# Kernel optimization log

Hardware: AMD Instinct MI355X
Metric: run time of the kernel (lower is better)

The kernel has to match this reference:

```python
import jax, jax.numpy as jnp
import numpy as np

HEADS = 16
NUM_LANDMARKS = 64
PINV_ITERS = 6
D_MODEL = 1024


def _moore_penrose_pinv(x, num_iters):
    # Newton-Schulz iteration: V <- 0.25*V @ (13I - KV @ (15I - KV @ (7I - KV)))
    m = x.shape[-1]
    I = jnp.eye(m, dtype=x.dtype)
    V = x
    for _ in range(num_iters):
        KV = x @ V  # [..., m, m]
        V = 0.25 * V @ (13.0 * I - KV @ (15.0 * I - KV @ (7.0 * I - KV)))
    return V


def setup_inputs() -> dict:
    key = jax.random.key(0)
    k1, k2, k3 = jax.random.split(key, 3)
    b, n, d = 4, 4096, D_MODEL
    hidden_states = jax.random.normal(k1, (b, n, d), dtype=jnp.float32)
    Wqkv = jax.random.normal(k2, (d, 3 * d), dtype=jnp.float32) * 0.02
    bqkv = jnp.zeros((3 * d,), dtype=jnp.float32)
    Wout = jax.random.normal(k3, (d, d), dtype=jnp.float32) * 0.02
    bout = jnp.zeros((d,), dtype=jnp.float32)
    return {"hidden_states": hidden_states, "Wqkv": Wqkv, "bqkv": bqkv,
            "Wout": Wout, "bout": bout}


def reference(hidden_states, Wqkv, bqkv, Wout, bout):
    b, n, d = hidden_states.shape
    h, m = HEADS, NUM_LANDMARKS
    dh = d // h
    scale = 1.0 / np.sqrt(dh).astype(np.float32)
    # n is a multiple of m by construction, so the torch padding branch is a no-op.
    l = n // m  # tokens per landmark group

    qkv = hidden_states @ Wqkv + bqkv  # [b, n, 3d]
    q, k, v = jnp.split(qkv, 3, axis=-1)

    def to_heads(t):  # [b, n, d] -> [b, h, n, dh]
        return t.reshape(b, n, h, dh).transpose(0, 2, 1, 3)

    q, k, v = to_heads(q), to_heads(k), to_heads(v)
    q = q * scale

    # Landmarks: mean over contiguous groups of l tokens (sum / l in original).
    q_l = q.reshape(b, h, m, l, dh).mean(axis=3)  # [b, h, m, dh]
    k_l = k.reshape(b, h, m, l, dh).mean(axis=3)

    sim1 = jnp.einsum('bhid,bhjd->bhij', q, k_l)    # [b, h, n, m]
    sim2 = jnp.einsum('bhid,bhjd->bhij', q_l, k_l)  # [b, h, m, m]
    sim3 = jnp.einsum('bhid,bhjd->bhij', q_l, k)    # [b, h, m, n]

    attn1 = jax.nn.softmax(sim1, axis=-1)
    attn2 = jax.nn.softmax(sim2, axis=-1)
    attn3 = jax.nn.softmax(sim3, axis=-1)

    attn2_inv = _moore_penrose_pinv(attn2, PINV_ITERS)

    # out = attn1 @ attn2_inv @ (attn3 @ v), cheapest association
    out = attn1 @ (attn2_inv @ (attn3 @ v))  # [b, h, n, dh]
    out = out.transpose(0, 2, 1, 3).reshape(b, n, d)
    out = out @ Wout + bout
    return out
```

## Files before the change

### kernel.cpp

```cpp
#include <hip/hip_runtime.h>
#include <cstdint>

typedef unsigned short u16;
typedef __attribute__((ext_vector_type(8))) short s16x8;
typedef __attribute__((ext_vector_type(4))) float f32x4;

#define NTOK 4096
#define DH   64
#define DM   1024
#define NH   16

static __device__ __forceinline__ float b2f(u16 u){ return __uint_as_float(((unsigned)u)<<16); }
static __device__ __forceinline__ u16 f2b(float f){
  unsigned u = __float_as_uint(f);
  return (u16)((u + 0x7FFFu + ((u>>16)&1u)) >> 16);
}

static __device__ __forceinline__ void gload_lds16(const void* g, void* l) {
  __builtin_amdgcn_global_load_lds(
      (const __attribute__((address_space(1))) unsigned*)(uintptr_t)g,
      (__attribute__((address_space(3))) unsigned*)(uintptr_t)l, 16, 0, 0);
}

static __device__ __forceinline__ s16x8 ld8(const u16* p){ return *(const s16x8*)(const void*)p; }

__global__ __launch_bounds__(256) void k_pre(const float* __restrict__ hs, u16* __restrict__ Xb,
                                             float* __restrict__ Xl,
                                             const float* __restrict__ Wqkv, u16* __restrict__ WqkvT,
                                             const float* __restrict__ Wout, u16* __restrict__ WoutT) {
  __shared__ float tile[64][65];
  const int bid = blockIdx.x, t = threadIdx.x;
  if (bid < 1024) {
    const int grp = bid >> 2;
    const int d = (bid & 3)*256 + t;
    const float* p = hs + (long)grp*64*DM + d;
    u16* xo = Xb + (long)grp*64*DM + d;
    float s = 0.f;
    #pragma unroll 8
    for (int i = 0; i < 64; ++i) {
      const float v = p[(long)i*DM];
      s += v;
      xo[(long)i*DM] = f2b(v);
    }
    Xl[(long)grp*DM + d] = s * (1.0f/64.0f);
    return;
  }
  const float* in; u16* out; int R, C, tc, tr;
  if (bid < 1792) { const int x = bid - 1024; in = Wqkv; out = WqkvT; R = 1024; C = 3072; tc = x % 48; tr = x / 48; }
  else            { const int x = bid - 1792; in = Wout; out = WoutT; R = 1024; C = 1024; tc = x & 15;  tr = x >> 4; }
  const int cx = t & 63, ry = t >> 6;
  #pragma unroll
  for (int p = 0; p < 16; ++p) {
    const int row = p*4 + ry;
    tile[row][cx] = in[(long)(tr*64 + row)*C + tc*64 + cx];
  }
  __syncthreads();
  #pragma unroll
  for (int p = 0; p < 16; ++p) {
    const int orow = p*4 + ry;
    out[(long)(tc*64 + orow)*R + tr*64 + cx] = f2b(tile[cx][orow]);
  }
}

__global__ __launch_bounds__(256) void k_lproj2(const float* __restrict__ Xl, const float* __restrict__ Wqkv,
                                                float* __restrict__ psum) {
  __shared__ __align__(16) float Xs[32][68];
  const int t = threadIdx.x;
  const int wcol = blockIdx.x*256 + t;
  const int r0 = blockIdx.y*32;
  const int kbase = blockIdx.z*128;
  float acc[32];
  #pragma unroll
  for (int r = 0; r < 32; ++r) acc[r] = 0.f;
  for (int k0 = kbase; k0 < kbase + 128; k0 += 64) {
    __syncthreads();
    for (int idx = t; idx < 2048; idx += 256)
      Xs[idx>>6][idx&63] = Xl[(long)(r0 + (idx>>6))*DM + k0 + (idx&63)];
    __syncthreads();
    for (int kk = 0; kk < 64; kk += 4) {
      f32x4 wv;
      #pragma unroll
      for (int j = 0; j < 4; ++j) wv[j] = Wqkv[(long)(k0+kk+j)*3072 + wcol];
      #pragma unroll
      for (int r = 0; r < 32; ++r) {
        const f32x4 xv = *(const f32x4*)&Xs[r][kk];
        acc[r] += xv[0]*wv[0] + xv[1]*wv[1] + xv[2]*wv[2] + xv[3]*wv[3];
      }
    }
  }
  float* po = psum + ((long)blockIdx.z*256 + r0)*2048 + wcol;
  #pragma unroll
  for (int r = 0; r < 32; ++r) po[(long)r*2048] = acc[r];
}

__global__ __launch_bounds__(256) void k_lreduce(const float* __restrict__ psum, const float* __restrict__ bqkv,
                                                 float* __restrict__ qlf, float* __restrict__ klf,
                                                 u16* __restrict__ qlb, u16* __restrict__ klb) {
  const long idx = (long)blockIdx.x*256 + threadIdx.x;
  const int row = (int)(idx >> 11), col = (int)(idx & 2047);
  float s = 0.f;
  #pragma unroll
  for (int z = 0; z < 8; ++z) s += psum[((long)z*256 + row)*2048 + col];
  const int isq = (col < 1024) ? 1 : 0;
  float val = s + bqkv[col];
  if (isq) val *= 0.125f;
  const int b = row >> 6, lm = row & 63;
  const int c2 = col & 1023, h = c2 >> 6, dh = c2 & 63;
  const long o = (((long)b*NH + h)*64 + lm)*64 + dh;
  if (isq) { qlf[o] = val; qlb[o] = f2b(val); }
  else     { klf[o] = val; klb[o] = f2b(val); }
}

template<int EPI>
__global__ __launch_bounds__(512, 2) void k_gemm256(
    const u16* __restrict__ A, const u16* __restrict__ Bt, const float* __restrict__ bias,
    int N, float* __restrict__ outF, u16* __restrict__ outQ, u16* __restrict__ outK, u16* __restrict__ outV)
{
  __shared__ __align__(16) u16 lds[2*32768];
  const int t = threadIdx.x;
  const int lane = t & 63;
  const int wid = t >> 6;
  const int c = lane & 15, g = lane >> 4;
  const int wm = wid >> 2, wn = wid & 3;
  const int fid = blockIdx.y*64 + blockIdx.x;
  const int nbx = ((fid & 7) << 3) | ((fid >> 3) & 7);
  const int nby = fid >> 6;
  const long arow0 = (long)nbx * 256;
  const long brow0 = (long)nby * 256;
  char* ldsb = (char*)lds;

  const int srow3 = t >> 3;
  const int sch = ((t & 7) ^ (srow3 & 7)) * 8;
  const u16* sA = A  + (arow0 + srow3)*1024 + sch;
  const u16* sB = Bt + (brow0 + srow3)*1024 + sch;
  const int dbase = t*16;

#define STG(gp, R0, Toff, kbe, nb) { \
    char* d0 = ldsb + (nb)*65536 + (Toff) + (R0)*128 + dbase; \
    gload_lds16((gp) + (long)(R0)*1024 + (kbe), d0); \
    gload_lds16((gp) + (long)((R0)+64)*1024 + (kbe), d0 + 8192); }

  const int cp0 = ((g     ) ^ (c & 7)) * 16;
  const int cp1 = ((4 | g ) ^ (c & 7)) * 16;
  int rowA[4], rowB[4];
  #pragma unroll
  for (int mi = 0; mi < 4; ++mi) {
    rowA[mi] = (wm*64 + mi*16 + c)*128;
    rowB[mi] = 32768 + (wn*64 + mi*16 + c)*128;
  }

  f32x4 acc0[4][4] = {};
  f32x4 acc1[4][4] = {};

  STG(sB, 0, 32768, 0, 0)
  STG(sB, 128, 32768, 0, 0)
  STG(sA, 0, 0, 0, 0)
  STG(sA, 128, 0, 0, 0)
  asm volatile("s_waitcnt vmcnt(2)" ::: "memory");
  __builtin_amdgcn_s_barrier();

  for (int it = 0; it < 16; ++it) {
    char* buf = ldsb + (it&1)*65536;
    const int nb = (it+1)&1;
    const int kb1 = (it+1)*64;
    const bool last = (it == 15);
    s16x8 fa[4], fb[4], ga[4];
    #pragma unroll
    for (int mi = 0; mi < 4; ++mi) fa[mi] = *(const s16x8*)(buf + rowA[mi] + cp0);
    #pragma unroll
    for (int ni = 0; ni < 4; ++ni) fb[ni] = *(const s16x8*)(buf + rowB[ni] + cp0);
    if (!last) STG(sB, 0, 32768, kb1, nb)
    __builtin_amdgcn_s_barrier();
    asm volatile("s_waitcnt lgkmcnt(0)" ::: "memory");
    __builtin_amdgcn_sched_barrier(0);
    __builtin_amdgcn_s_setprio(1);
    #pragma unroll
    for (int mi = 0; mi < 4; ++mi)
      #pragma unroll
      for (int ni = 0; ni < 4; ++ni)
        acc0[mi][ni] = __builtin_amdgcn_mfma_f32_16x16x32_bf16(fa[mi], fb[ni], acc0[mi][ni], 0, 0, 0);
    __builtin_amdgcn_s_setprio(0);
    if (last) { asm volatile("s_waitcnt vmcnt(0)" ::: "memory"); }
    else      { asm volatile("s_waitcnt vmcnt(2)" ::: "memory"); }
    __builtin_amdgcn_s_barrier();
    #pragma unroll
    for (int mi = 0; mi < 4; ++mi) ga[mi] = *(const s16x8*)(buf + rowA[mi] + 16384 + cp0);
    if (!last) STG(sB, 128, 32768, kb1, nb)
    __builtin_amdgcn_s_barrier();
    asm volatile("s_waitcnt lgkmcnt(0)" ::: "memory");
    __builtin_amdgcn_sched_barrier(0);
    __builtin_amdgcn_s_setprio(1);
    #pragma unroll
    for (int mi = 0; mi < 4; ++mi)
      #pragma unroll
      for (int ni = 0; ni < 4; ++ni)
        acc1[mi][ni] = __builtin_amdgcn_mfma_f32_16x16x32_bf16(ga[mi], fb[ni], acc1[mi][ni], 0, 0, 0);
    __builtin_amdgcn_s_setprio(0);
    __builtin_amdgcn_s_barrier();
    #pragma unroll
    for (int mi = 0; mi < 4; ++mi) fa[mi] = *(const s16x8*)(buf + rowA[mi] + cp1);
    #pragma unroll
    for (int ni = 0; ni < 4; ++ni) fb[ni] = *(const s16x8*)(buf + rowB[ni] + cp1);
    if (!last) STG(sA, 0, 0, kb1, nb)
    __builtin_amdgcn_s_barrier();
    asm volatile("s_waitcnt lgkmcnt(0)" ::: "memory");
    __builtin_amdgcn_sched_barrier(0);
    __builtin_amdgcn_s_setprio(1);
    #pragma unroll
    for (int mi = 0; mi < 4; ++mi)
      #pragma unroll
      for (int ni = 0; ni < 4; ++ni)
        acc0[mi][ni] = __builtin_amdgcn_mfma_f32_16x16x32_bf16(fa[mi], fb[ni], acc0[mi][ni], 0, 0, 0);
    __builtin_amdgcn_s_setprio(0);
    __builtin_amdgcn_s_barrier();
    #pragma unroll
    for (int mi = 0; mi < 4; ++mi) ga[mi] = *(const s16x8*)(buf + rowA[mi] + 16384 + cp1);
    if (!last) STG(sA, 128, 0, kb1, nb)
    __builtin_amdgcn_s_barrier();
    asm volatile("s_waitcnt lgkmcnt(0)" ::: "memory");
    __builtin_amdgcn_sched_barrier(0);
    __builtin_amdgcn_s_setprio(1);
    #pragma unroll
    for (int mi = 0; mi < 4; ++mi)
      #pragma unroll
      for (int ni = 0; ni < 4; ++ni)
        acc1[mi][ni] = __builtin_amdgcn_mfma_f32_16x16x32_bf16(ga[mi], fb[ni], acc1[mi][ni], 0, 0, 0);
    __builtin_amdgcn_s_setprio(0);
    if (!last) { asm volatile("s_waitcnt vmcnt(2)" ::: "memory"); }
    __builtin_amdgcn_s_barrier();
  }
#undef STG

  if (EPI == 0) {
    const int tensor = (int)(brow0 >> 10);
    if (tensor == 2) {
      __syncthreads();
      u16* wlds = lds + wid*4224;
      const int hbase = (int)((brow0 + wn*64) & 1023);
      const int head = hbase >> 6;
      #pragma unroll
      for (int ph = 0; ph < 2; ++ph) {
        const long grow0 = arow0 + ph*128 + wm*64;
        const int b = (int)(grow0 >> 12), tok0r = (int)(grow0 & 4095);
        #pragma unroll
        for (int mi = 0; mi < 4; ++mi)
          #pragma unroll
          for (int ni = 0; ni < 4; ++ni) {
            const float bv = bias[brow0 + wn*64 + ni*16 + c];
            const f32x4 a = ph ? acc1[mi][ni] : acc0[mi][ni];
            #pragma unroll
            for (int r = 0; r < 4; ++r)
              wlds[(mi*16 + g*4 + r)*66 + ni*16 + c] = f2b(a[r] + bv);
          }
        asm volatile("s_waitcnt lgkmcnt(0)" ::: "memory");
        u16* vbase = outV + (((long)b*NH + head)*DH)*NTOK + tok0r;
        #pragma unroll
        for (int j = 0; j < 8; ++j) {
          const int d = j*8 + (lane >> 3);
          const int tk = (lane & 7)*8;
          s16x8 vv;
          #pragma unroll
          for (int s2 = 0; s2 < 8; ++s2) vv[s2] = (short)wlds[(tk + s2)*66 + d];
          *(s16x8*)(vbase + (long)d*NTOK + tk) = vv;
        }
        asm volatile("s_waitcnt lgkmcnt(0)" ::: "memory");
      }
    } else {
      u16* dst = (tensor == 0) ? outQ : outK;
      const float mul = (tensor == 0) ? 0.125f : 1.0f;
      #pragma unroll
      for (int ph = 0; ph < 2; ++ph)
        #pragma unroll
        for (int mi = 0; mi < 4; ++mi) {
          const int rowb = ph*128 + wm*64 + mi*16 + g*4;
          #pragma unroll
          for (int ni = 0; ni < 4; ++ni) {
            const long gcol = brow0 + wn*64 + ni*16 + c;
            const int c2 = (int)(gcol & 1023);
            const int head = c2 >> 6, dh = c2 & 63;
            const float bv = bias[gcol];
            const f32x4 a = ph ? acc1[mi][ni] : acc0[mi][ni];
            #pragma unroll
            for (int r = 0; r < 4; ++r) {
              const long grow = arow0 + rowb + r;
              const int b = (int)(grow >> 12), tok = (int)(grow & 4095);
              dst[(((long)b*NH + head)*NTOK + tok)*DH + dh] = f2b((a[r] + bv)*mul);
            }
          }
        }
    }
  } else {
    #pragma unroll
    for (int ph = 0; ph < 2; ++ph)
      #pragma unroll
      for (int mi = 0; mi < 4; ++mi) {
        const int rowb = ph*128 + wm*64 + mi*16 + g*4;
        #pragma unroll
        for (int ni = 0; ni < 4; ++ni) {
          const long gcol = brow0 + wn*64 + ni*16 + c;
          const float bv = bias[gcol];
          const f32x4 a = ph ? acc1[mi][ni] : acc0[mi][ni];
          #pragma unroll
          for (int r = 0; r < 4; ++r) {
            const long grow = arow0 + rowb + r;
            outF[grow*N + gcol] = a[r] + bv;
          }
        }
      }
  }
}

#define PST 68
static __device__ __forceinline__ void mm_nn8(const float* A, const float* B, float* C, int t) {
  const int lane = t & 63, j0 = (t >> 6) << 3;
  float acc[8];
  #pragma unroll
  for (int j = 0; j < 8; ++j) acc[j] = 0.f;
  for (int k = 0; k < 64; k += 4) {
    const f32x4 a4 = *(const f32x4*)&A[lane*PST + k];
    #pragma unroll
    for (int dk = 0; dk < 4; ++dk) {
      const float a = a4[dk];
      const float* br = &B[(k + dk)*PST + j0];
      const f32x4 b0 = *(const f32x4*)(br);
      const f32x4 b1 = *(const f32x4*)(br + 4);
      #pragma unroll
      for (int qq = 0; qq < 4; ++qq) { acc[qq] += a*b0[qq]; acc[4+qq] += a*b1[qq]; }
    }
  }
  #pragma unroll
  for (int j = 0; j < 8; ++j) C[lane*PST + j0 + j] = acc[j];
}
static __device__ __forceinline__ void mm_nt8(const float* A, const float* B, float* C, int t) {
  const int lane = t & 63, j0 = (t >> 6) << 3;
  float acc[8];
  #pragma unroll
  for (int j = 0; j < 8; ++j) acc[j] = 0.f;
  for (int k = 0; k < 64; k += 4) {
    const f32x4 a4 = *(const f32x4*)&A[lane*PST + k];
    #pragma unroll
    for (int jj = 0; jj < 8; ++jj) {
      const f32x4 b4 = *(const f32x4*)&B[(j0 + jj)*PST + k];
      acc[jj] += a4[0]*b4[0] + a4[1]*b4[1] + a4[2]*b4[2] + a4[3]*b4[3];
    }
  }
  #pragma unroll
  for (int j = 0; j < 8; ++j) C[lane*PST + j0 + j] = acc[j];
}
static __device__ __forceinline__ void mm_nn4(const float* A, const float* B, float* C, int t) {
  const int lane = t & 63, j0 = (t >> 6) << 2;
  float acc[4] = {0.f, 0.f, 0.f, 0.f};
  for (int k = 0; k < 64; k += 4) {
    const f32x4 a4 = *(const f32x4*)&A[lane*PST + k];
    #pragma unroll
    for (int dk = 0; dk < 4; ++dk) {
      const f32x4 b0 = *(const f32x4*)&B[(k + dk)*PST + j0];
      #pragma unroll
      for (int q = 0; q < 4; ++q) acc[q] += a4[dk]*b0[q];
    }
  }
  #pragma unroll
  for (int j = 0; j < 4; ++j) C[lane*PST + j0 + j] = acc[j];
}

__global__ __launch_bounds__(512) void k_pa(const float* __restrict__ qlf, const float* __restrict__ klf,
                                            float* __restrict__ a2inv,
                                            const u16* __restrict__ qlb, const u16* __restrict__ kk,
                                            const u16* __restrict__ vt,
                                            float* __restrict__ zp, float* __restrict__ sp) {
  __shared__ __align__(16) char smem[87040];
  const int t = threadIdx.x;
  if (blockIdx.x < 64) {
    float* Xb = (float*)smem;
    float* Vb = Xb + 64*PST;
    float* T1 = Vb + 64*PST;
    float* T2 = T1 + 64*PST;
    float* T3 = T2 + 64*PST;
    const int bh = blockIdx.x;
    const float* ql = qlf + (long)bh*4096;
    const float* kl = klf + (long)bh*4096;
    for (int i = t; i < 4096; i += 512) { T1[(i>>6)*PST + (i&63)] = ql[i]; T2[(i>>6)*PST + (i&63)] = kl[i]; }
    __syncthreads();
    mm_nt8(T1, T2, Xb, t);
    __syncthreads();
    if (t < 64) {
      float mx = -1e30f;
      for (int j = 0; j < 64; ++j) mx = fmaxf(mx, Xb[t*PST + j]);
      float s = 0.f;
      for (int j = 0; j < 64; ++j) { const float e = expf(Xb[t*PST + j] - mx); Xb[t*PST + j] = e; s += e; }
      const float inv = 1.0f/s;
      for (int j = 0; j < 64; ++j) Xb[t*PST + j] *= inv;
    }
    __syncthreads();
    for (int i = t; i < 4096; i += 512) { const int r = i>>6, cc = i&63; Vb[r*PST+cc] = Xb[r*PST+cc]; }
    __syncthreads();
    for (int it = 0; it < 6; ++it) {
      mm_nn8(Xb, Vb, T1, t);  __syncthreads();
      for (int i = t; i < 4096; i += 512) { const int r=i>>6, cc=i&63; T2[r*PST+cc] = (r==cc?7.0f:0.0f) - T1[r*PST+cc]; }
      __syncthreads();
      mm_nn8(T1, T2, T3, t);  __syncthreads();
      for (int i = t; i < 4096; i += 512) { const int r=i>>6, cc=i&63; T2[r*PST+cc] = (r==cc?15.0f:0.0f) - T3[r*PST+cc]; }
      __syncthreads();
      mm_nn8(T1, T2, T3, t);  __syncthreads();
      for (int i = t; i < 4096; i += 512) { const int r=i>>6, cc=i&63; T2[r*PST+cc] = (r==cc?13.0f:0.0f) - T3[r*PST+cc]; }
      __syncthreads();
      mm_nn8(Vb, T2, T3, t);  __syncthreads();
      for (int i = t; i < 4096; i += 512) { const int r=i>>6, cc=i&63; Vb[r*PST+cc] = 0.25f*T3[r*PST+cc]; }
      __syncthreads();
    }
    for (int i = t; i < 4096; i += 512) a2inv[(long)bh*4096 + i] = Vb[(i>>6)*PST + (i&63)];
    return;
  }
  float* Zlp = (float*)smem;
  float* Slp = (float*)(smem + 65536);
  char*  Plb = smem + 66560;
  const int abid = blockIdx.x - 64;
  const int bh = abid >> 3, qt = abid & 7;
  if (t < 256) {
    const int w = t >> 6, lane = t & 63;
    const int c = lane & 15, g = lane >> 4;
    s16x8 aq[4][2];
    const u16* qlp = qlb + (long)bh*4096;
    #pragma unroll
    for (int mi = 0; mi < 4; ++mi)
      #pragma unroll
      for (int ks = 0; ks < 2; ++ks)
        aq[mi][ks] = ld8(qlp + (mi*16 + c)*64 + ks*32 + g*8);

    f32x4 zacc[4][4] = {};
    float sl[4][4] = {};
    const u16* kp = kk + (long)bh*NTOK*DH;
    const u16* vp = vt + (long)bh*DH*NTOK;
    char* pbase = Plb + w*5120;
    const int tok00 = qt*512 + w*128;

    for (int it = 0; it < 4; ++it) {
      const int t0 = tok00 + it*32;
      f32x4 sacc[4][2] = {};
      s16x8 kb[2][2];
      #pragma unroll
      for (int cg = 0; cg < 2; ++cg)
        #pragma unroll
        for (int ks = 0; ks < 2; ++ks)
          kb[cg][ks] = ld8(kp + (long)(t0 + cg*16 + c)*64 + ks*32 + g*8);
      #pragma unroll
      for (int cg = 0; cg < 2; ++cg)
        #pragma unroll
        for (int ks = 0; ks < 2; ++ks)
          #pragma unroll
          for (int mi = 0; mi < 4; ++mi)
            sacc[mi][cg] = __builtin_amdgcn_mfma_f32_16x16x32_bf16(aq[mi][ks], kb[cg][ks], sacc[mi][cg], 0, 0, 0);
      #pragma unroll
      for (int mi = 0; mi < 4; ++mi)
        #pragma unroll
        for (int r = 0; r < 4; ++r) {
          const int row = mi*16 + g*4 + r;
          const float p0 = __expf(sacc[mi][0][r]);
          const float p1 = __expf(sacc[mi][1][r]);
          sl[mi][r] += p0 + p1;
          char* base = pbase + row*80;
          *(u16*)(base + c*2)      = f2b(p0);
          *(u16*)(base + 32 + c*2) = f2b(p1);
        }
      s16x8 pa[4];
      #pragma unroll
      for (int mi = 0; mi < 4; ++mi) pa[mi] = *(const s16x8*)(pbase + (mi*16 + c)*80 + g*16);
      #pragma unroll
      for (int ni = 0; ni < 4; ++ni) {
        const s16x8 vb = ld8(vp + (long)(ni*16 + c)*NTOK + t0 + g*8);
        #pragma unroll
        for (int mi = 0; mi < 4; ++mi)
          zacc[mi][ni] = __builtin_amdgcn_mfma_f32_16x16x32_bf16(pa[mi], vb, zacc[mi][ni], 0, 0, 0);
      }
    }
    #pragma unroll
    for (int mi = 0; mi < 4; ++mi)
      #pragma unroll
      for (int r = 0; r < 4; ++r) {
        float s = sl[mi][r];
        s += __shfl_xor(s, 1); s += __shfl_xor(s, 2); s += __shfl_xor(s, 4); s += __shfl_xor(s, 8);
        sl[mi][r] = s;
      }
    #pragma unroll
    for (int mi = 0; mi < 4; ++mi)
      #pragma unroll
      for (int ni = 0; ni < 4; ++ni)
        #pragma unroll
        for (int r = 0; r < 4; ++r)
          Zlp[w*4096 + (mi*16 + g*4 + r)*64 + ni*16 + c] = zacc[mi][ni][r];
    if (c == 0)
      #pragma unroll
      for (int mi = 0; mi < 4; ++mi)
        #pragma unroll
        for (int r = 0; r < 4; ++r)
          Slp[w*64 + mi*16 + g*4 + r] = sl[mi][r];
  }
  __syncthreads();
  float* zpp = zp + (long)abid*4096;
  for (int i = t; i < 4096; i += 512)
    zpp[i] = Zlp[i] + Zlp[4096 + i] + Zlp[8192 + i] + Zlp[12288 + i];
  if (t < 64) sp[(long)abid*64 + t] = Slp[t] + Slp[64 + t] + Slp[128 + t] + Slp[192 + t];
}

__global__ __launch_bounds__(1024) void k_w2(const float* __restrict__ a2inv,
                                             const float* __restrict__ zp, const float* __restrict__ sp,
                                             u16* __restrict__ w2t) {
  __shared__ __align__(16) float Ai[64*PST];
  __shared__ __align__(16) float Zi[64*PST];
  __shared__ __align__(16) float Ci[64*PST];
  __shared__ float Ss[64];
  const int bh = blockIdx.x, t = threadIdx.x;
  if (t < 64) {
    float ss = 0.f;
    #pragma unroll
    for (int qt = 0; qt < 8; ++qt) ss += sp[(long)(bh*8 + qt)*64 + t];
    Ss[t] = 1.0f / ss;
  }
  for (int i = t; i < 4096; i += 1024)
    Ai[(i>>6)*PST + (i&63)] = a2inv[(long)bh*4096 + i];
  __syncthreads();
  for (int i = t; i < 4096; i += 1024) {
    float zs = 0.f;
    #pragma unroll
    for (int qt = 0; qt < 8; ++qt) zs += zp[((long)(bh*8 + qt))*4096 + i];
    Zi[(i>>6)*PST + (i&63)] = zs * Ss[i>>6];
  }
  __syncthreads();
  mm_nn4(Ai, Zi, Ci, t);
  __syncthreads();
  for (int i = t; i < 4096; i += 1024) { const int r = i>>6, cc = i&63; w2t[(long)bh*4096 + cc*64 + r] = f2b(Ci[r*PST + cc]); }
}

#define P1ST 144
__global__ __launch_bounds__(256) void k_attn1(const u16* __restrict__ q, const u16* __restrict__ klb,
                                               const u16* __restrict__ w2t, u16* __restrict__ ao) {
  __shared__ __align__(16) u16 Pl[4][64][72];
  const int bx = blockIdx.x, bh = bx >> 4, tt = bx & 15;
  const int b = bh >> 4, h = bh & 15;
  const int t = threadIdx.x, w = t >> 6, lane = t & 63;
  const int c = lane & 15, g = lane >> 4;
  const int tok0 = tt*256 + w*64;
  const u16* qp  = q + ((long)bh*NTOK + tok0)*DH;
  const u16* klp = klb + (long)bh*4096;
  const u16* wp  = w2t + (long)bh*4096;
  char* pbase = (char*)&Pl[w][0][0];

  s16x8 aq[4][2], kb[4][2], wb[4][2];
  #pragma unroll
  for (int i = 0; i < 4; ++i)
    #pragma unroll
    for (int ks = 0; ks < 2; ++ks) {
      aq[i][ks] = ld8(qp + (long)(i*16 + c)*DH + ks*32 + g*8);
      kb[i][ks] = ld8(klp + (i*16 + c)*64 + ks*32 + g*8);
      wb[i][ks] = ld8(wp  + (i*16 + c)*64 + ks*32 + g*8);
    }
  f32x4 sacc[4][4] = {};
  #pragma unroll
  for (int ks = 0; ks < 2; ++ks)
    #pragma unroll
    for (int mi = 0; mi < 4; ++mi)
      #pragma unroll
      for (int ni = 0; ni < 4; ++ni)
        sacc[mi][ni] = __builtin_amdgcn_mfma_f32_16x16x32_bf16(aq[mi][ks], kb[ni][ks], sacc[mi][ni], 0, 0, 0);

  float rs[4][4];
  #pragma unroll
  for (int mi = 0; mi < 4; ++mi)
    #pragma unroll
    for (int r = 0; r < 4; ++r) {
      const int row = mi*16 + g*4 + r;
      char* base = pbase + row*P1ST;
      float ssum = 0.f;
      #pragma unroll
      for (int ni = 0; ni < 4; ++ni) {
        const float p = __expf(sacc[mi][ni][r]);
        ssum += p;
        *(u16*)(base + (ni*16 + c)*2) = f2b(p);
      }
      ssum += __shfl_xor(ssum, 1); ssum += __shfl_xor(ssum, 2);
      ssum += __shfl_xor(ssum, 4); ssum += __shfl_xor(ssum, 8);
      rs[mi][r] = ssum;
    }
  __builtin_amdgcn_s_barrier();
  s16x8 pa[4][2];
  #pragma unroll
  for (int mi = 0; mi < 4; ++mi)
    #pragma unroll
    for (int ks = 0; ks < 2; ++ks)
      pa[mi][ks] = *(const s16x8*)(pbase + (mi*16 + c)*P1ST + ks*64 + g*16);
  f32x4 oacc[4][4] = {};
  #pragma unroll
  for (int ks = 0; ks < 2; ++ks)
    #pragma unroll
    for (int mi = 0; mi < 4; ++mi)
      #pragma unroll
      for (int ni = 0; ni < 4; ++ni)
        oacc[mi][ni] = __builtin_amdgcn_mfma_f32_16x16x32_bf16(pa[mi][ks], wb[ni][ks], oacc[mi][ni], 0, 0, 0);

  u16* op = ao + (long)b*NTOK*DM + (long)h*64;
  #pragma unroll
  for (int mi = 0; mi < 4; ++mi)
    #pragma unroll
    for (int r = 0; r < 4; ++r) {
      const int tok = tok0 + mi*16 + g*4 + r;
      const float inv = 1.0f / rs[mi][r];
      #pragma unroll
      for (int ni = 0; ni < 4; ++ni)
        op[(long)tok*DM + ni*16 + c] = f2b(oacc[mi][ni][r] * inv);
    }
}

extern "C" void kernel_launch(void* const* d_in, const int* in_sizes, int n_in,
                              void* d_out, int out_size, void* d_ws, size_t ws_size,
                              hipStream_t stream) {
  const float* hs   = (const float*)d_in[0];
  const float* Wqkv = (const float*)d_in[1];
  const float* bqkv = (const float*)d_in[2];
  const float* Wout = (const float*)d_in[3];
  const float* bout = (const float*)d_in[4];
  float* out = (float*)d_out;
  char* w = (char*)d_ws;

  u16*  Xb    = (u16*)(w);
  float* zp   = (float*)(w);
  float* sp   = (float*)(w + 8388608L);
  u16*  WqkvT = (u16*)(w + 33554432L);
  u16*  WoutT = (u16*)(w + 39845888L);
  u16*  q     = (u16*)(w + 41943040L);
  float* psum = (float*)(w + 41943040L);
  u16*  k     = (u16*)(w + 75497472L);
  float* Xl   = (float*)(w + 109051904L);
  u16*  vt    = (u16*)(w + 142606336L);
  float* qlf  = (float*)(w + 176160768L);
  float* klf  = (float*)(w + 177209344L);
  u16*  qlb   = (u16*)(w + 178257920L);
  u16*  klb   = (u16*)(w + 178782208L);
  float* a2i  = (float*)(w + 179306496L);
  u16*  w2t   = (u16*)(w + 181403648L);
  u16*  ao    = (u16*)(w + 181927936L);

  k_pre<<<2048, 256, 0, stream>>>(hs, Xb, Xl, Wqkv, WqkvT, Wout, WoutT);
  k_lproj2<<<dim3(8,8,8), 256, 0, stream>>>(Xl, Wqkv, psum);
  k_lreduce<<<2048, 256, 0, stream>>>(psum, bqkv, qlf, klf, qlb, klb);
  k_gemm256<0><<<dim3(64,12), 512, 0, stream>>>(Xb, WqkvT, bqkv, 3072, nullptr, q, k, vt);
  k_pa<<<576, 512, 0, stream>>>(qlf, klf, a2i, qlb, k, vt, zp, sp);
  k_w2<<<64, 1024, 0, stream>>>(a2i, zp, sp, w2t);
  k_attn1<<<1024, 256, 0, stream>>>(q, klb, w2t, ao);
  k_gemm256<1><<<dim3(64,4), 512, 0, stream>>>(ao, WoutT, bout, 1024, out, nullptr, nullptr, nullptr);
}
```

Measured before the change: 324.9 us.

## Widen pinv blocks to 1024 threads and loop attn1 over token tiles

The k_pa kernel now launches 1024 threads. The Newton-Schulz pinv matmuls switch to 4-column-per-thread variants (mm_nn4/mm_nt4), so 16 waves share the 64x64 products instead of 8. k_attn1 now runs 256 blocks that each loop over four 256-token tiles, reusing the landmark K and W2 fragments held in registers across tiles, and replaces the block barrier with an LDS waitcnt because each wave's scratch is private. The aim is shorter serial latency in the pinv chain and fewer redundant fragment loads in attn1. The cost is that non-pinv k_pa blocks leave 768 threads idle, and attn1 exposes far less block-level parallelism.

```diff
diff --git a/kernel.cpp b/kernel.cpp
--- a/kernel.cpp
+++ b/kernel.cpp
@@ -311,42 +311,6 @@
 }
 
 #define PST 68
-static __device__ __forceinline__ void mm_nn8(const float* A, const float* B, float* C, int t) {
-  const int lane = t & 63, j0 = (t >> 6) << 3;
-  float acc[8];
-  #pragma unroll
-  for (int j = 0; j < 8; ++j) acc[j] = 0.f;
-  for (int k = 0; k < 64; k += 4) {
-    const f32x4 a4 = *(const f32x4*)&A[lane*PST + k];
-    #pragma unroll
-    for (int dk = 0; dk < 4; ++dk) {
-      const float a = a4[dk];
-      const float* br = &B[(k + dk)*PST + j0];
-      const f32x4 b0 = *(const f32x4*)(br);
-      const f32x4 b1 = *(const f32x4*)(br + 4);
-      #pragma unroll
-      for (int qq = 0; qq < 4; ++qq) { acc[qq] += a*b0[qq]; acc[4+qq] += a*b1[qq]; }
-    }
-  }
-  #pragma unroll
-  for (int j = 0; j < 8; ++j) C[lane*PST + j0 + j] = acc[j];
-}
-static __device__ __forceinline__ void mm_nt8(const float* A, const float* B, float* C, int t) {
-  const int lane = t & 63, j0 = (t >> 6) << 3;
-  float acc[8];
-  #pragma unroll
-  for (int j = 0; j < 8; ++j) acc[j] = 0.f;
-  for (int k = 0; k < 64; k += 4) {
-    const f32x4 a4 = *(const f32x4*)&A[lane*PST + k];
-    #pragma unroll
-    for (int jj = 0; jj < 8; ++jj) {
-      const f32x4 b4 = *(const f32x4*)&B[(j0 + jj)*PST + k];
-      acc[jj] += a4[0]*b4[0] + a4[1]*b4[1] + a4[2]*b4[2] + a4[3]*b4[3];
-    }
-  }
-  #pragma unroll
-  for (int j = 0; j < 8; ++j) C[lane*PST + j0 + j] = acc[j];
-}
 static __device__ __forceinline__ void mm_nn4(const float* A, const float* B, float* C, int t) {
   const int lane = t & 63, j0 = (t >> 6) << 2;
   float acc[4] = {0.f, 0.f, 0.f, 0.f};
@@ -362,12 +326,26 @@
   #pragma unroll
   for (int j = 0; j < 4; ++j) C[lane*PST + j0 + j] = acc[j];
 }
-
-__global__ __launch_bounds__(512) void k_pa(const float* __restrict__ qlf, const float* __restrict__ klf,
-                                            float* __restrict__ a2inv,
-                                            const u16* __restrict__ qlb, const u16* __restrict__ kk,
-                                            const u16* __restrict__ vt,
-                                            float* __restrict__ zp, float* __restrict__ sp) {
+static __device__ __forceinline__ void mm_nt4(const float* A, const float* B, float* C, int t) {
+  const int lane = t & 63, j0 = (t >> 6) << 2;
+  float acc[4] = {0.f, 0.f, 0.f, 0.f};
+  for (int k = 0; k < 64; k += 4) {
+    const f32x4 a4 = *(const f32x4*)&A[lane*PST + k];
+    #pragma unroll
+    for (int jj = 0; jj < 4; ++jj) {
+      const f32x4 b4 = *(const f32x4*)&B[(j0 + jj)*PST + k];
+      acc[jj] += a4[0]*b4[0] + a4[1]*b4[1] + a4[2]*b4[2] + a4[3]*b4[3];
+    }
+  }
+  #pragma unroll
+  for (int j = 0; j < 4; ++j) C[lane*PST + j0 + j] = acc[j];
+}
+
+__global__ __launch_bounds__(1024) void k_pa(const float* __restrict__ qlf, const float* __restrict__ klf,
+                                             float* __restrict__ a2inv,
+                                             const u16* __restrict__ qlb, const u16* __restrict__ kk,
+                                             const u16* __restrict__ vt,
+                                             float* __restrict__ zp, float* __restrict__ sp) {
   __shared__ __align__(16) char smem[87040];
   const int t = threadIdx.x;
   if (blockIdx.x < 64) {
@@ -379,9 +357,9 @@
     const int bh = blockIdx.x;
     const float* ql = qlf + (long)bh*4096;
     const float* kl = klf + (long)bh*4096;
-    for (int i = t; i < 4096; i += 512) { T1[(i>>6)*PST + (i&63)] = ql[i]; T2[(i>>6)*PST + (i&63)] = kl[i]; }
+    for (int i = t; i < 4096; i += 1024) { T1[(i>>6)*PST + (i&63)] = ql[i]; T2[(i>>6)*PST + (i&63)] = kl[i]; }
     __syncthreads();
-    mm_nt8(T1, T2, Xb, t);
+    mm_nt4(T1, T2, Xb, t);
     __syncthreads();
     if (t < 64) {
       float mx = -1e30f;
@@ -392,23 +370,23 @@
       for (int j = 0; j < 64; ++j) Xb[t*PST + j] *= inv;
     }
     __syncthreads();
-    for (int i = t; i < 4096; i += 512) { const int r = i>>6, cc = i&63; Vb[r*PST+cc] = Xb[r*PST+cc]; }
+    for (int i = t; i < 4096; i += 1024) { const int r = i>>6, cc = i&63; Vb[r*PST+cc] = Xb[r*PST+cc]; }
     __syncthreads();
     for (int it = 0; it < 6; ++it) {
-      mm_nn8(Xb, Vb, T1, t);  __syncthreads();
-      for (int i = t; i < 4096; i += 512) { const int r=i>>6, cc=i&63; T2[r*PST+cc] = (r==cc?7.0f:0.0f) - T1[r*PST+cc]; }
+      mm_nn4(Xb, Vb, T1, t);  __syncthreads();
+      for (int i = t; i < 4096; i += 1024) { const int r=i>>6, cc=i&63; T2[r*PST+cc] = (r==cc?7.0f:0.0f) - T1[r*PST+cc]; }
       __syncthreads();
-      mm_nn8(T1, T2, T3, t);  __syncthreads();
-      for (int i = t; i < 4096; i += 512) { const int r=i>>6, cc=i&63; T2[r*PST+cc] = (r==cc?15.0f:0.0f) - T3[r*PST+cc]; }
+      mm_nn4(T1, T2, T3, t);  __syncthreads();
+      for (int i = t; i < 4096; i += 1024) { const int r=i>>6, cc=i&63; T2[r*PST+cc] = (r==cc?15.0f:0.0f) - T3[r*PST+cc]; }
       __syncthreads();
-      mm_nn8(T1, T2, T3, t);  __syncthreads();
-      for (int i = t; i < 4096; i += 512) { const int r=i>>6, cc=i&63; T2[r*PST+cc] = (r==cc?13.0f:0.0f) - T3[r*PST+cc]; }
+      mm_nn4(T1, T2, T3, t);  __syncthreads();
+      for (int i = t; i < 4096; i += 1024) { const int r=i>>6, cc=i&63; T2[r*PST+cc] = (r==cc?13.0f:0.0f) - T3[r*PST+cc]; }
       __syncthreads();
-      mm_nn8(Vb, T2, T3, t);  __syncthreads();
-      for (int i = t; i < 4096; i += 512) { const int r=i>>6, cc=i&63; Vb[r*PST+cc] = 0.25f*T3[r*PST+cc]; }
+      mm_nn4(Vb, T2, T3, t);  __syncthreads();
+      for (int i = t; i < 4096; i += 1024) { const int r=i>>6, cc=i&63; Vb[r*PST+cc] = 0.25f*T3[r*PST+cc]; }
       __syncthreads();
     }
-    for (int i = t; i < 4096; i += 512) a2inv[(long)bh*4096 + i] = Vb[(i>>6)*PST + (i&63)];
+    for (int i = t; i < 4096; i += 1024) a2inv[(long)bh*4096 + i] = Vb[(i>>6)*PST + (i&63)];
     return;
   }
   float* Zlp = (float*)smem;
@@ -497,7 +475,7 @@
   }
   __syncthreads();
   float* zpp = zp + (long)abid*4096;
-  for (int i = t; i < 4096; i += 512)
+  for (int i = t; i < 4096; i += 1024)
     zpp[i] = Zlp[i] + Zlp[4096 + i] + Zlp[8192 + i] + Zlp[12288 + i];
   if (t < 64) sp[(long)abid*64 + t] = Slp[t] + Slp[64 + t] + Slp[128 + t] + Slp[192 + t];
 }
@@ -535,79 +513,88 @@
 __global__ __launch_bounds__(256) void k_attn1(const u16* __restrict__ q, const u16* __restrict__ klb,
                                                const u16* __restrict__ w2t, u16* __restrict__ ao) {
   __shared__ __align__(16) u16 Pl[4][64][72];
-  const int bx = blockIdx.x, bh = bx >> 4, tt = bx & 15;
+  const int bx = blockIdx.x, bh = bx >> 2, qd = bx & 3;
   const int b = bh >> 4, h = bh & 15;
   const int t = threadIdx.x, w = t >> 6, lane = t & 63;
   const int c = lane & 15, g = lane >> 4;
-  const int tok0 = tt*256 + w*64;
-  const u16* qp  = q + ((long)bh*NTOK + tok0)*DH;
   const u16* klp = klb + (long)bh*4096;
   const u16* wp  = w2t + (long)bh*4096;
   char* pbase = (char*)&Pl[w][0][0];
 
-  s16x8 aq[4][2], kb[4][2], wb[4][2];
+  s16x8 kb[4][2], wb[4][2];
   #pragma unroll
   for (int i = 0; i < 4; ++i)
     #pragma unroll
     for (int ks = 0; ks < 2; ++ks) {
-      aq[i][ks] = ld8(qp + (long)(i*16 + c)*DH + ks*32 + g*8);
       kb[i][ks] = ld8(klp + (i*16 + c)*64 + ks*32 + g*8);
       wb[i][ks] = ld8(wp  + (i*16 + c)*64 + ks*32 + g*8);
     }
-  f32x4 sacc[4][4] = {};
-  #pragma unroll
-  for (int ks = 0; ks < 2; ++ks)
-    #pragma unroll
-    for (int mi = 0; mi < 4; ++mi)
-      #pragma unroll
-      for (int ni = 0; ni < 4; ++ni)
-        sacc[mi][ni] = __builtin_amdgcn_mfma_f32_16x16x32_bf16(aq[mi][ks], kb[ni][ks], sacc[mi][ni], 0, 0, 0);
-
-  float rs[4][4];
-  #pragma unroll
-  for (int mi = 0; mi < 4; ++mi)
-    #pragma unroll
-    for (int r = 0; r < 4; ++r) {
-      const int row = mi*16 + g*4 + r;
-      char* base = pbase + row*P1ST;
-      float ssum = 0.f;
-      #pragma unroll
-      for (int ni = 0; ni < 4; ++ni) {
-        const float p = __expf(sacc[mi][ni][r]);
-        ssum += p;
-        *(u16*)(base + (ni*16 + c)*2) = f2b(p);
+  u16* op = ao + (long)b*NTOK*DM + (long)h*64;
+
+  for (int tt = 0; tt < 4; ++tt) {
+    const int tok0 = qd*1024 + tt*256 + w*64;
+    const u16* qp = q + ((long)bh*NTOK + tok0)*DH;
+    s16x8 aq[4][2];
+    #pragma unroll
+    for (int i = 0; i < 4; ++i)
+      #pragma unroll
+      for (int ks = 0; ks < 2; ++ks)
+        aq[i][ks] = ld8(qp + (long)(i*16 + c)*DH + ks*32 + g*8);
+    f32x4 sacc[4][4] = {};
+    #pragma unroll
+    for (int ks = 0; ks < 2; ++ks)
+      #pragma unroll
+      for (int mi = 0; mi < 4; ++mi)
+        #pragma unroll
+        for (int ni = 0; ni < 4; ++ni)
+          sacc[mi][ni] = __builtin_amdgcn_mfma_f32_16x16x32_bf16(aq[mi][ks], kb[ni][ks], sacc[mi][ni], 0, 0, 0);
+
+    float rs[4][4];
+    #pragma unroll
+    for (int mi = 0; mi < 4; ++mi)
+      #pragma unroll
+      for (int r = 0; r < 4; ++r) {
+        const int row = mi*16 + g*4 + r;
+        char* base = pbase + row*P1ST;
+        float ssum = 0.f;
+        #pragma unroll
+        for (int ni = 0; ni < 4; ++ni) {
+          const float p = __expf(sacc[mi][ni][r]);
+          ssum += p;
+          *(u16*)(base + (ni*16 + c)*2) = f2b(p);
+        }
+        ssum += __shfl_xor(ssum, 1); ssum += __shfl_xor(ssum, 2);
+        ssum += __shfl_xor(ssum, 4); ssum += __shfl_xor(ssum, 8);
+        rs[mi][r] = ssum;
       }
-      ssum += __shfl_xor(ssum, 1); ssum += __shfl_xor(ssum, 2);
-      ssum += __shfl_xor(ssum, 4); ssum += __shfl_xor(ssum, 8);
-      rs[mi][r] = ssum;
-    }
-  __builtin_amdgcn_s_barrier();
-  s16x8 pa[4][2];
-  #pragma unroll
-  for (int mi = 0; mi < 4; ++mi)
+    asm volatile("s_waitcnt lgkmcnt(0)" ::: "memory");
+    s16x8 pa[4][2];
+    #pragma unroll
+    for (int mi = 0; mi < 4; ++mi)
+      #pragma unroll
+      for (int ks = 0; ks < 2; ++ks)
+        pa[mi][ks] = *(const s16x8*)(pbase + (mi*16 + c)*P1ST + ks*64 + g*16);
+    f32x4 oacc[4][4] = {};
     #pragma unroll
     for (int ks = 0; ks < 2; ++ks)
-      pa[mi][ks] = *(const s16x8*)(pbase + (mi*16 + c)*P1ST + ks*64 + g*16);
-  f32x4 oacc[4][4] = {};
-  #pragma unroll
-  for (int ks = 0; ks < 2; ++ks)
-    #pragma unroll
-    for (int mi = 0; mi < 4; ++mi)
-      #pragma unroll
-      for (int ni = 0; ni < 4; ++ni)
-        oacc[mi][ni] = __builtin_amdgcn_mfma_f32_16x16x32_bf16(pa[mi][ks], wb[ni][ks], oacc[mi][ni], 0, 0, 0);
-
-  u16* op = ao + (long)b*NTOK*DM + (long)h*64;
-  #pragma unroll
-  for (int mi = 0; mi < 4; ++mi)
-    #pragma unroll
-    for (int r = 0; r < 4; ++r) {
-      const int tok = tok0 + mi*16 + g*4 + r;
-      const float inv = 1.0f / rs[mi][r];
-      #pragma unroll
-      for (int ni = 0; ni < 4; ++ni)
-        op[(long)tok*DM + ni*16 + c] = f2b(oacc[mi][ni][r] * inv);
-    }
+      #pragma unroll
+      for (int mi = 0; mi < 4; ++mi)
+        #pragma unroll
+        for (int ni = 0; ni < 4; ++ni)
+          oacc[mi][ni] = __builtin_amdgcn_mfma_f32_16x16x32_bf16(pa[mi][ks], wb[ni][ks], oacc[mi][ni], 0, 0, 0);
+
+    #pragma unroll
+    for (int mi = 0; mi < 4; ++mi)
+      #pragma unroll
+      for (int r = 0; r < 4; ++r) {
+        const int tok = tok0 + mi*16 + g*4 + r;
+        const float inv = 1.0f / rs[mi][r];
+        #pragma unroll
+        for (int ni = 0; ni < 4; ++ni)
+          op[(long)tok*DM + ni*16 + c] = f2b(oacc[mi][ni][r] * inv);
+      }
+    asm volatile("s_waitcnt lgkmcnt(0)" ::: "memory");
+  }
 }
 
 extern "C" void kernel_launch(void* const* d_in, const int* in_sizes, int n_in,
@@ -643,8 +630,8 @@
   k_lproj2<<<dim3(8,8,8), 256, 0, stream>>>(Xl, Wqkv, psum);
   k_lreduce<<<2048, 256, 0, stream>>>(psum, bqkv, qlf, klf, qlb, klb);
   k_gemm256<0><<<dim3(64,12), 512, 0, stream>>>(Xb, WqkvT, bqkv, 3072, nullptr, q, k, vt);
-  k_pa<<<576, 512, 0, stream>>>(qlf, klf, a2i, qlb, k, vt, zp, sp);
+  k_pa<<<576, 1024, 0, stream>>>(qlf, klf, a2i, qlb, k, vt, zp, sp);
   k_w2<<<64, 1024, 0, stream>>>(a2i, zp, sp, w2t);
-  k_attn1<<<1024, 256, 0, stream>>>(q, klb, w2t, ao);
+  k_attn1<<<256, 256, 0, stream>>>(q, klb, w2t, ao);
   k_gemm256<1><<<dim3(64,4), 512, 0, stream>>>(ao, WoutT, bout, 1024, out, nullptr, nullptr, nullptr);
 }
```

Measured after the change: 352.3 us. 1.08x slower.
